# Kernel optimization log

Hardware: AMD Instinct MI355X
Metric: run time of the kernel (lower is better)

## Reference

```python
import jax, jax.numpy as jnp
import numpy as np
from jax import lax

N, M, B = 512, 1024, 1024  # signal dim, atoms, batch (batch==m required by X = W @ Gamma)
POWER_ITER = 100
IHT_ITER = 50


def setup_inputs() -> dict:
    key = jax.random.key(0)
    k1, k2 = jax.random.split(key)
    Y = jax.random.normal(k1, (B, N), dtype=jnp.float32)
    W = jax.random.normal(k2, (N, M), dtype=jnp.float32)
    return {"Y": Y, "W": W, "K": 64}


def power_method(W):
    # 100 iterations of X <- X W^T W / ||.||; returns last pre-normalization norm
    # (approx largest eigenvalue of W^T W), matching PowerMethod in the source.
    X0 = jax.random.normal(jax.random.key(42), (1, W.shape[1]), dtype=W.dtype)

    def body(i, carry):
        X, _ = carry
        X2 = (X @ W.T) @ W          # [1, m]
        nm = jnp.linalg.norm(X2)
        return (X2 / nm, nm)

    _, nm = lax.fori_loop(0, POWER_ITER, body, (X0, jnp.asarray(1.0, W.dtype)))
    return nm


def hard_threshold_k(G, K):
    # keep entries strictly larger (in abs) than the (K+1)-th largest per row
    a = jnp.sort(jnp.abs(G), axis=1)[:, ::-1]   # descending per row
    T = a[:, K][:, None]                          # [B, 1]
    return G * (jnp.abs(G) > T).astype(G.dtype)


def reference(Y, W, K):
    # NormDict: column-normalize the dictionary
    W = W / jnp.linalg.norm(W, axis=0)
    c = power_method(W)
    eta = 1.0 / c
    Yn = jnp.linalg.norm(Y)

    # IHT sparse coding
    Gamma = hard_threshold_k(Y @ (eta * W), K)     # [B, m]
    residual = Gamma @ W.T - Y                      # [B, n]

    def step(carry, _):
        Gamma, residual = carry
        Gamma = hard_threshold_k(Gamma - eta * (residual @ W), K)
        residual = Gamma @ W.T - Y
        return (Gamma, residual), jnp.linalg.norm(residual) / Yn

    (Gamma, residual), norms = lax.scan(step, (Gamma, residual), None, length=IHT_ITER)

    X = W @ Gamma  # [n, m] @ [B, m] -> requires B == m, as in the torch source
    return X, Gamma, norms
```

## Files before the change

### kernel.cpp

```cpp
#include <hip/hip_runtime.h>


#define DEV __device__ __forceinline__

constexpr int Nd = 512;
constexpr int Md = 1024;
constexpr int Bd = 1024;
constexpr int Ksp = 64;
constexpr int IHT = 50;

DEV float wave_reduce_f(float v) {
#pragma unroll
  for (int off = 32; off > 0; off >>= 1) v += __shfl_down(v, off);
  return v;
}
DEV double wave_reduce_d(double v) {
#pragma unroll
  for (int off = 32; off > 0; off >>= 1) v += __shfl_down(v, off);
  return v;
}
DEV float rfl_f(float v) {
  return __uint_as_float(__builtin_amdgcn_readfirstlane(__float_as_uint(v)));
}

__global__ void k_zero(double* dacc, int* pcnt) {
  int t = threadIdx.x;
  if (t < 51) dacc[t] = 0.0;
  if (t < 52) pcnt[t] = 0;
}

__global__ __launch_bounds__(256) void k_colnorm(const float* __restrict__ W,
                                                 float* __restrict__ cnorm) {
  int col = blockIdx.x * 256 + threadIdx.x;
  double ss = 0.0;
  for (int i = 0; i < Nd; ++i) {
    float w = W[(size_t)i * Md + col];
    ss = fma((double)w, (double)w, ss);
  }
  cnorm[col] = (float)sqrt(ss);
}

__global__ __launch_bounds__(256) void k_normalize(const float* __restrict__ W,
                                                   const float* __restrict__ cnorm,
                                                   float* __restrict__ Wn) {
  int idx = blockIdx.x * 256 + threadIdx.x;
  Wn[idx] = W[idx] / cnorm[idx & (Md - 1)];
}

__global__ __launch_bounds__(256) void k_yn2(const float* __restrict__ Y,
                                             double* __restrict__ dacc) {
  double s = 0.0;
  for (int i = blockIdx.x * 256 + threadIdx.x; i < Bd * Nd; i += gridDim.x * 256) {
    float y = Y[i];
    s = fma((double)y, (double)y, s);
  }
  s = wave_reduce_d(s);
  __shared__ double red[4];
  int lane = threadIdx.x & 63, wid = threadIdx.x >> 6;
  if (lane == 0) red[wid] = s;
  __syncthreads();
  if (threadIdx.x == 0) atomicAdd(&dacc[0], red[0] + red[1] + red[2] + red[3]);
}

template <int BM, int BN, int TN>
__global__ __launch_bounds__(256) void k_gemm_t(const float* __restrict__ A, int lda, int ta,
                                                const float* __restrict__ B, int ldb, int tb,
                                                float* __restrict__ C, int ldc, int Kd,
                                                float scale) {
  constexpr int AE = 32 * BM / 256;
  constexpr int BE = 32 * BN / 256;
  __shared__ __align__(16) float As[32][BM + 4];
  __shared__ __align__(16) float Bs[32][BN + 4];
  const int tid = threadIdx.x;
  const int tx = tid % (BN / TN), ty = tid / (BN / TN);
  const int m0 = blockIdx.y * BM, n0 = blockIdx.x * BN;
  float ra[AE], rb[BE];
  float acc[4][TN];
#pragma unroll
  for (int i = 0; i < 4; ++i)
#pragma unroll
    for (int j = 0; j < TN; ++j) acc[i][j] = 0.f;

  auto loadA = [&](int k0) {
    if (!ta) {
      const int c = tid & 31, r0 = tid >> 5;
#pragma unroll
      for (int i = 0; i < AE; ++i)
        ra[i] = A[(size_t)(m0 + r0 + i * 8) * lda + (k0 + c)];
    } else {
      const int r = tid % BM, c0 = tid / BM;
#pragma unroll
      for (int i = 0; i < AE; ++i)
        ra[i] = A[(size_t)(k0 + c0 + i * (256 / BM)) * lda + (m0 + r)];
    }
  };
  auto storeA = [&]() {
    if (!ta) {
      const int c = tid & 31, r0 = tid >> 5;
#pragma unroll
      for (int i = 0; i < AE; ++i) As[c][r0 + i * 8] = ra[i];
    } else {
      const int r = tid % BM, c0 = tid / BM;
#pragma unroll
      for (int i = 0; i < AE; ++i) As[c0 + i * (256 / BM)][r] = ra[i];
    }
  };
  auto loadB = [&](int k0) {
    if (!tb) {
      const int c = tid % BN, r0 = tid / BN;
#pragma unroll
      for (int i = 0; i < BE; ++i)
        rb[i] = B[(size_t)(k0 + r0 + i * (256 / BN)) * ldb + (n0 + c)];
    } else {
      const int r = tid & 31, c0 = tid >> 5;
#pragma unroll
      for (int i = 0; i < BE; ++i)
        rb[i] = B[(size_t)(n0 + c0 + i * 8) * ldb + (k0 + r)];
    }
  };
  auto storeB = [&]() {
    if (!tb) {
      const int c = tid % BN, r0 = tid / BN;
#pragma unroll
      for (int i = 0; i < BE; ++i) Bs[r0 + i * (256 / BN)][c] = rb[i];
    } else {
      const int r = tid & 31, c0 = tid >> 5;
#pragma unroll
      for (int i = 0; i < BE; ++i) Bs[r][c0 + i * 8] = rb[i];
    }
  };

  loadA(0);
  loadB(0);
  storeA();
  storeB();
  __syncthreads();
  for (int k0 = 0; k0 < Kd; k0 += 32) {
    const bool more = (k0 + 32) < Kd;
    if (more) { loadA(k0 + 32); loadB(k0 + 32); }
#pragma unroll
    for (int kk = 0; kk < 32; ++kk) {
      const float4 a4 = *(const float4*)&As[kk][ty * 4];
      const float aa[4] = {a4.x, a4.y, a4.z, a4.w};
      float bb[TN];
      if constexpr (TN == 4) {
        const float4 b4 = *(const float4*)&Bs[kk][tx * 4];
        bb[0] = b4.x; bb[1] = b4.y; bb[2] = b4.z; bb[3] = b4.w;
      } else {
        const float2 b2 = *(const float2*)&Bs[kk][tx * 2];
        bb[0] = b2.x; bb[1] = b2.y;
      }
#pragma unroll
      for (int i = 0; i < 4; ++i)
#pragma unroll
        for (int j = 0; j < TN; ++j) acc[i][j] = fmaf(aa[i], bb[j], acc[i][j]);
    }
    if (more) {
      __syncthreads();
      storeA();
      storeB();
      __syncthreads();
    }
  }
#pragma unroll
  for (int i = 0; i < 4; ++i) {
    if constexpr (TN == 4) {
      float4 o;
      o.x = acc[i][0] * scale; o.y = acc[i][1] * scale;
      o.z = acc[i][2] * scale; o.w = acc[i][3] * scale;
      *(float4*)&C[(size_t)(m0 + ty * 4 + i) * ldc + n0 + tx * 4] = o;
    } else {
      float2 o;
      o.x = acc[i][0] * scale; o.y = acc[i][1] * scale;
      *(float2*)&C[(size_t)(m0 + ty * 4 + i) * ldc + n0 + tx * 2] = o;
    }
  }
}

DEV float erfinv_xla(float x) {
  float w = -log1pf(-x * x);
  float p;
  if (w < 5.0f) {
    w = w - 2.5f;
    p = 2.81022636e-08f;
    p = fmaf(p, w, 3.43273939e-07f);
    p = fmaf(p, w, -3.5233877e-06f);
    p = fmaf(p, w, -4.39150654e-06f);
    p = fmaf(p, w, 0.00021858087f);
    p = fmaf(p, w, -0.00125372503f);
    p = fmaf(p, w, -0.00417768164f);
    p = fmaf(p, w, 0.246640727f);
    p = fmaf(p, w, 1.50140941f);
  } else {
    w = sqrtf(w) - 3.0f;
    p = -0.000200214257f;
    p = fmaf(p, w, 0.000100950558f);
    p = fmaf(p, w, 0.00134934322f);
    p = fmaf(p, w, -0.00367342844f);
    p = fmaf(p, w, 0.00573950773f);
    p = fmaf(p, w, -0.0076224613f);
    p = fmaf(p, w, 0.00943887047f);
    p = fmaf(p, w, 1.00167406f);
    p = fmaf(p, w, 2.83297682f);
  }
  return p * x;
}

#define TF_ROUND(r)                                  \
  {                                                  \
    x0 += x1;                                        \
    x1 = (x1 << (r)) | (x1 >> (32 - (r)));           \
    x1 ^= x0;                                        \
  }

__global__ __launch_bounds__(512) void k_power(const float* __restrict__ Wn,
                                               const float* __restrict__ S2,
                                               const float* __restrict__ Smat,
                                               float* __restrict__ V,
                                               float* __restrict__ cbuf,
                                               int* __restrict__ pcnt) {
  __shared__ float xbuf[Md];
  __shared__ double r99[8], r100[8];
  const int t = threadIdx.x, lane = t & 63, wv = t >> 6;
  const int bk = blockIdx.x;
  const int nblk = (int)gridDim.x;

  {
    unsigned i = (unsigned)t;
    unsigned x0 = i, x1 = i + 512u;
    const unsigned ks0 = 0u, ks1 = 42u, ks2 = 0x1BD11BDAu ^ 42u;
    x0 += ks0; x1 += ks1;
    TF_ROUND(13) TF_ROUND(15) TF_ROUND(26) TF_ROUND(6)  x0 += ks1; x1 += ks2 + 1u;
    TF_ROUND(17) TF_ROUND(29) TF_ROUND(16) TF_ROUND(24) x0 += ks2; x1 += ks0 + 2u;
    TF_ROUND(13) TF_ROUND(15) TF_ROUND(26) TF_ROUND(6)  x0 += ks0; x1 += ks1 + 3u;
    TF_ROUND(17) TF_ROUND(29) TF_ROUND(16) TF_ROUND(24) x0 += ks1; x1 += ks2 + 4u;
    TF_ROUND(13) TF_ROUND(15) TF_ROUND(26) TF_ROUND(6)  x0 += ks2; x1 += ks0 + 5u;
    const float lo = -0.99999994f;
    const float sqrt2 = 1.41421356237f;
    {
      float f = __uint_as_float((x0 >> 9) | 0x3f800000u) - 1.0f;
      float u = fmaxf(lo, f * 2.0f + lo);
      xbuf[i] = sqrt2 * erfinv_xla(u);
    }
    {
      float f = __uint_as_float((x1 >> 9) | 0x3f800000u) - 1.0f;
      float u = fmaxf(lo, f * 2.0f + lo);
      xbuf[i + 512] = sqrt2 * erfinv_xla(u);
    }
  }
  __syncthreads();

  float* s0 = V;
  float* s1 = V + 512;
  float* v99 = V + 1024;
  float* v100 = V + 1536;
  const int w = bk * 8 + wv;

  for (int i = 0; i < 8; ++i) {
    const int row = w + 64 * i;
    const float4* wr = (const float4*)(Wn + (size_t)row * Md);
    const float4* x4 = (const float4*)xbuf;
    float s = 0.f;
#pragma unroll
    for (int e = 0; e < 4; ++e) {
      const float4 w4 = wr[lane + e * 64];
      const float4 xx = x4[lane + e * 64];
      s = fmaf(w4.x, xx.x, s); s = fmaf(w4.y, xx.y, s);
      s = fmaf(w4.z, xx.z, s); s = fmaf(w4.w, xx.w, s);
    }
    s = wave_reduce_f(s);
    if (lane == 0) s0[row] = s;
  }
  __syncthreads();
  if (t == 0) {
    __hip_atomic_fetch_add(&pcnt[0], 1, __ATOMIC_RELEASE, __HIP_MEMORY_SCOPE_AGENT);
    while (__hip_atomic_load(&pcnt[0], __ATOMIC_ACQUIRE, __HIP_MEMORY_SCOPE_AGENT) < nblk) {}
  }
  __syncthreads();

  const float* pin = s0;
  for (int step = 0; step < 51; ++step) {
    const float* M;
    float scale;
    float* dst;
    if (step < 49)      { M = S2;   scale = 1.0f;   dst = (step & 1) ? s0 : s1; }
    else if (step == 49){ M = Smat; scale = 0.125f; dst = v99; }
    else                { M = Smat; scale = 0.125f; dst = v100; }
    for (int i = 0; i < 8; ++i) {
      const int row = w + 64 * i;
      const float4* mr = (const float4*)(M + (size_t)row * Nd);
      const float4* v4 = (const float4*)pin;
      float s = 0.f;
#pragma unroll
      for (int e = 0; e < 2; ++e) {
        const float4 m4 = mr[lane + e * 64];
        const float4 xx = v4[lane + e * 64];
        s = fmaf(m4.x, xx.x, s); s = fmaf(m4.y, xx.y, s);
        s = fmaf(m4.z, xx.z, s); s = fmaf(m4.w, xx.w, s);
      }
      s = wave_reduce_f(s);
      if (lane == 0) dst[row] = s * scale;
    }
    __syncthreads();
    if (t == 0) {
      __hip_atomic_fetch_add(&pcnt[1 + step], 1, __ATOMIC_RELEASE, __HIP_MEMORY_SCOPE_AGENT);
      while (__hip_atomic_load(&pcnt[1 + step], __ATOMIC_ACQUIRE, __HIP_MEMORY_SCOPE_AGENT) < nblk) {}
    }
    __syncthreads();
    pin = dst;
  }

  if (bk == 0) {
    double a = (double)v99[t]; a *= a;
    double b2 = (double)v100[t]; b2 *= b2;
    a = wave_reduce_d(a);
    b2 = wave_reduce_d(b2);
    if (lane == 0) { r99[wv] = a; r100[wv] = b2; }
    __syncthreads();
    if (t == 0) {
      double n99 = 0.0, n100 = 0.0;
      for (int i = 0; i < 8; ++i) { n99 += r99[i]; n100 += r100[i]; }
      float c = (float)(8.0 * sqrt(n100 / n99));
      cbuf[0] = c;
      cbuf[1] = 1.0f / c;
    }
  }
}

__global__ __launch_bounds__(256, 4) void k_iht_all(
    const float* __restrict__ Q, const float* __restrict__ YW,
    const float* __restrict__ cbuf, float* __restrict__ gdense,
    double* __restrict__ normacc) {
  __shared__ float u[Md];
  __shared__ float yws[Md];
  __shared__ float sval[Ksp];
  __shared__ int sidx[Ksp];
  __shared__ unsigned histbuf[2][4][256];
  __shared__ unsigned wred[4];
  __shared__ unsigned sel_need, sel_prefix;
  __shared__ double dred[4];
  __shared__ int scnt;

  const int t = threadIdx.x;
  const int b = blockIdx.x;
  const int lane = t & 63, wv = t >> 6;
  const float eta = cbuf[1];
  const float4 yw = ((const float4*)(YW + (size_t)b * Md))[t];
  ((float4*)yws)[t] = yw;
#pragma unroll
  for (int e = 0; e < 8; ++e) ((unsigned*)histbuf)[t + e * 256] = 0u;
  const float* Qt = Q + t * 4;

  for (int it = -1; it < IHT; ++it) {
    if (it >= 0) {
      const int cnt = scnt;
      float4 p = make_float4(0.f, 0.f, 0.f, 0.f);
      int k = 0;
      for (; k + 16 <= cnt; k += 16) {
        int ids[16];
        float gs[16];
        float4 qq[16];
#pragma unroll
        for (int j = 0; j < 16; ++j) {
          ids[j] = __builtin_amdgcn_readfirstlane(sidx[k + j]);
          gs[j] = rfl_f(sval[k + j]);
        }
#pragma unroll
        for (int j = 0; j < 16; ++j) qq[j] = *(const float4*)(Qt + (size_t)ids[j] * Md);
#pragma unroll
        for (int j = 0; j < 16; ++j) p.x = fmaf(gs[j], qq[j].x, p.x);
#pragma unroll
        for (int j = 0; j < 16; ++j) p.y = fmaf(gs[j], qq[j].y, p.y);
#pragma unroll
        for (int j = 0; j < 16; ++j) p.z = fmaf(gs[j], qq[j].z, p.z);
#pragma unroll
        for (int j = 0; j < 16; ++j) p.w = fmaf(gs[j], qq[j].w, p.w);
      }
      for (; k < cnt; ++k) {
        const int id = __builtin_amdgcn_readfirstlane(sidx[k]);
        const float g = rfl_f(sval[k]);
        const float4 q = *(const float4*)(Qt + (size_t)id * Md);
        p.x = fmaf(g, q.x, p.x); p.y = fmaf(g, q.y, p.y);
        p.z = fmaf(g, q.z, p.z); p.w = fmaf(g, q.w, p.w);
      }
      ((float4*)u)[t] = p;
      __syncthreads();
      if (it >= 1) {
        double part = 0.0;
        if (t < cnt) {
          const int id = sidx[t];
          part = (double)sval[t] * ((double)u[id] - 2.0 * (double)yws[id]);
        }
        part = wave_reduce_d(part);
        if (lane == 0) dred[wv] = part;
      }
      __syncthreads();
      if (it >= 1 && t == 0)
        atomicAdd(&normacc[it - 1], dred[0] + dred[1] + dred[2] + dred[3]);
      float4 uu;
      uu.x = -(eta * (p.x - yw.x)); uu.y = -(eta * (p.y - yw.y));
      uu.z = -(eta * (p.z - yw.z)); uu.w = -(eta * (p.w - yw.w));
      ((float4*)u)[t] = uu;
      __syncthreads();
      if (t < cnt) u[sidx[t]] += sval[t];
      __syncthreads();
    } else {
      float4 uu;
      uu.x = eta * yw.x; uu.y = eta * yw.y; uu.z = eta * yw.z; uu.w = eta * yw.w;
      ((float4*)u)[t] = uu;
      __syncthreads();
    }

    float vals[4];
    unsigned key[4];
    {
      const float4 mv = ((const float4*)u)[t];
      vals[0] = mv.x; vals[1] = mv.y; vals[2] = mv.z; vals[3] = mv.w;
#pragma unroll
      for (int e = 0; e < 4; ++e) key[e] = __float_as_uint(vals[e]) & 0x7fffffffu;
    }

    unsigned need = Ksp + 1, prefix = 0u, pmask = 0u;
#pragma unroll
    for (int pass = 3; pass >= 0; --pass) {
      const int sh = 8 * pass;
      const int pb = pass & 1;
      unsigned(*hist)[256] = histbuf[pb];
#pragma unroll
      for (int e = 0; e < 4; ++e)
        if ((key[e] & pmask) == prefix) atomicAdd(&hist[wv][(key[e] >> sh) & 255u], 1u);
      __syncthreads();
      unsigned* hz = histbuf[pb ^ 1][wv];
      hz[lane] = 0u; hz[lane + 64] = 0u; hz[lane + 128] = 0u; hz[lane + 192] = 0u;
      if (wv == 0) {
        const unsigned c0 = hist[0][lane] + hist[1][lane] + hist[2][lane] + hist[3][lane];
        const unsigned c1 = hist[0][lane + 64] + hist[1][lane + 64] + hist[2][lane + 64] + hist[3][lane + 64];
        const unsigned c2 = hist[0][lane + 128] + hist[1][lane + 128] + hist[2][lane + 128] + hist[3][lane + 128];
        const unsigned c3 = hist[0][lane + 192] + hist[1][lane + 192] + hist[2][lane + 192] + hist[3][lane + 192];
        unsigned s0 = c0, s1 = c1, s2 = c2, s3 = c3;
#pragma unroll
        for (int off = 1; off < 64; off <<= 1) {
          const unsigned y0 = __shfl_down(s0, off), y1 = __shfl_down(s1, off);
          const unsigned y2 = __shfl_down(s2, off), y3 = __shfl_down(s3, off);
          if (lane + off < 64) { s0 += y0; s1 += y1; s2 += y2; s3 += y3; }
        }
        const unsigned T1 = __builtin_amdgcn_readfirstlane(s1);
        const unsigned T2 = __builtin_amdgcn_readfirstlane(s2);
        const unsigned T3 = __builtin_amdgcn_readfirstlane(s3);
        const unsigned i0 = s0 + T1 + T2 + T3;
        const unsigned i1 = s1 + T2 + T3;
        const unsigned i2 = s2 + T3;
        const unsigned i3 = s3;
        if (i0 >= need && i0 - c0 < need) { sel_prefix = prefix | ((unsigned)lane << sh); sel_need = need - (i0 - c0); }
        if (i1 >= need && i1 - c1 < need) { sel_prefix = prefix | ((unsigned)(lane + 64) << sh); sel_need = need - (i1 - c1); }
        if (i2 >= need && i2 - c2 < need) { sel_prefix = prefix | ((unsigned)(lane + 128) << sh); sel_need = need - (i2 - c2); }
        if (i3 >= need && i3 - c3 < need) { sel_prefix = prefix | ((unsigned)(lane + 192) << sh); sel_need = need - (i3 - c3); }
      }
      __syncthreads();
      prefix = sel_prefix;
      need = sel_need;
      pmask |= (255u << sh);
    }
    const unsigned Tbits = prefix;

    unsigned keep = 0u;
    unsigned myc = 0u;
#pragma unroll
    for (int e = 0; e < 4; ++e)
      if (key[e] > Tbits) { keep |= (1u << e); ++myc; }
    unsigned x = myc;
#pragma unroll
    for (int off = 1; off < 64; off <<= 1) {
      const unsigned y = __shfl_up(x, off);
      if (lane >= off) x += y;
    }
    if (lane == 63) wred[wv] = x;
    __syncthreads();
    unsigned addlo = 0u;
    for (int w2 = 0; w2 < wv; ++w2) addlo += wred[w2];
    int base = (int)(x + addlo) - (int)myc;
#pragma unroll
    for (int e = 0; e < 4; ++e) {
      if (keep & (1u << e)) {
        sidx[base] = t * 4 + e;
        sval[base] = vals[e];
        ++base;
      }
    }
    if (t == 0) scnt = (int)(wred[0] + wred[1] + wred[2] + wred[3]);
    if (it == IHT - 1) {
      float4 g;
      g.x = (keep & 1u) ? vals[0] : 0.f;
      g.y = (keep & 2u) ? vals[1] : 0.f;
      g.z = (keep & 4u) ? vals[2] : 0.f;
      g.w = (keep & 8u) ? vals[3] : 0.f;
      ((float4*)(gdense + (size_t)b * Md))[t] = g;
    }
    __syncthreads();
  }

  const int cnt = scnt;
  if (wv == 0) {
    double part = 0.0;
    if (lane < cnt) {
      const int id = sidx[lane];
      float acc2 = 0.f;
      for (int k = 0; k < cnt; ++k)
        acc2 = fmaf(sval[k], Q[(size_t)sidx[k] * Md + id], acc2);
      part = (double)sval[lane] * ((double)acc2 - 2.0 * (double)yws[id]);
    }
    part = wave_reduce_d(part);
    if (lane == 0) atomicAdd(&normacc[IHT - 1], part);
  }
}

__global__ void k_wnorms(const double* __restrict__ dacc, float* __restrict__ onorms) {
  const int t = threadIdx.x;
  if (t < IHT) {
    const double yn2 = dacc[0];
    double r2 = yn2 + dacc[1 + t];
    if (r2 < 0.0) r2 = 0.0;
    onorms[t] = (float)(sqrt(r2) / sqrt(yn2));
  }
}

extern "C" void kernel_launch(void* const* d_in, const int* in_sizes, int n_in,
                              void* d_out, int out_size, void* d_ws, size_t ws_size,
                              hipStream_t stream) {
  (void)in_sizes; (void)n_in; (void)out_size; (void)ws_size;
  const float* Y = (const float*)d_in[0];
  const float* W = (const float*)d_in[1];
  float* out = (float*)d_out;
  float* outX = out;
  float* outG = out + Nd * Md;
  float* outN = outG + Bd * Md;

  char* wsb = (char*)d_ws;
  double* dacc = (double*)wsb;
  float* cbuf = (float*)(wsb + 512);
  float* Wn = (float*)(wsb + 1024);
  float* Q = Wn + Nd * Md;
  float* YW = Q + Md * Md;
  float* Smat = YW + Bd * Md;
  float* S2 = Smat + Nd * Nd;
  float* cnorm = S2 + Nd * Nd;
  float* V = cnorm + Md;
  int* pcnt = (int*)(V + 2048);

  k_zero<<<1, 64, 0, stream>>>(dacc, pcnt);
  k_colnorm<<<4, 256, 0, stream>>>(W, cnorm);
  k_normalize<<<2048, 256, 0, stream>>>(W, cnorm, Wn);

  k_gemm_t<64, 32, 2><<<dim3(16, 8), 256, 0, stream>>>(Wn, Md, 0, Wn, Md, 1, Smat, Nd, Md, 1.0f);
  k_gemm_t<64, 32, 2><<<dim3(16, 8), 256, 0, stream>>>(Smat, Nd, 0, Smat, Nd, 0, S2, Nd, Nd, 0.015625f);
  k_gemm_t<64, 64, 4><<<dim3(16, 16), 256, 0, stream>>>(Wn, Md, 1, Wn, Md, 0, Q, Md, Nd, 1.0f);
  k_gemm_t<64, 64, 4><<<dim3(16, 16), 256, 0, stream>>>(Y, Nd, 0, Wn, Md, 0, YW, Md, Nd, 1.0f);
  k_yn2<<<128, 256, 0, stream>>>(Y, dacc);

  k_power<<<8, 512, 0, stream>>>(Wn, S2, Smat, V, cbuf, pcnt);

  k_iht_all<<<1024, 256, 0, stream>>>(Q, YW, cbuf, outG, dacc + 1);
  k_wnorms<<<1, 64, 0, stream>>>(dacc, outN);

  k_gemm_t<64, 32, 2><<<dim3(32, 8), 256, 0, stream>>>(Wn, Md, 0, outG, Md, 0, outX, Md, Md, 1.0f);
}
```

Measured before the change: 1.066 ms.

## Replace atomic-counter grid barrier with per-block flags and double power blocks

The persistent power-iteration kernel now uses a flag-based grid barrier. Each block publishes a monotonically increasing step value in its own padded slot, and one wavefront polls all slots with a wave-wide vote. This replaces a shared atomic counter per step. The block count goes from 8 to 16, so each wave handles 4 rows instead of 8, aiming to shorten each of the 51 serialized steps. The trade-off is more blocks taking part in every barrier, and the zeroing kernel is widened to clear the padded flag array.

```diff
diff --git a/kernel.cpp b/kernel.cpp
--- a/kernel.cpp
+++ b/kernel.cpp
@@ -8,6 +8,7 @@
 constexpr int Bd = 1024;
 constexpr int Ksp = 64;
 constexpr int IHT = 50;
+constexpr int NBLK = 16;
 
 DEV float wave_reduce_f(float v) {
 #pragma unroll
@@ -23,10 +24,10 @@
   return __uint_as_float(__builtin_amdgcn_readfirstlane(__float_as_uint(v)));
 }
 
-__global__ void k_zero(double* dacc, int* pcnt) {
+__global__ __launch_bounds__(512) void k_zero(double* dacc, int* pcnt) {
   int t = threadIdx.x;
   if (t < 51) dacc[t] = 0.0;
-  if (t < 52) pcnt[t] = 0;
+  pcnt[t] = 0;
 }
 
 __global__ __launch_bounds__(256) void k_colnorm(const float* __restrict__ W,
@@ -223,7 +224,24 @@
   __shared__ double r99[8], r100[8];
   const int t = threadIdx.x, lane = t & 63, wv = t >> 6;
   const int bk = blockIdx.x;
-  const int nblk = (int)gridDim.x;
+
+  auto flag_barrier = [&](int val) {
+    __syncthreads();
+    if (t == 0)
+      __hip_atomic_store(&pcnt[bk * 32], val, __ATOMIC_RELEASE,
+                         __HIP_MEMORY_SCOPE_AGENT);
+    if (wv == 0) {
+      while (true) {
+        int f = (lane < NBLK)
+                    ? __hip_atomic_load(&pcnt[lane * 32], __ATOMIC_ACQUIRE,
+                                        __HIP_MEMORY_SCOPE_AGENT)
+                    : val;
+        if (__all(f >= val)) break;
+        __builtin_amdgcn_s_sleep(1);
+      }
+    }
+    __syncthreads();
+  };
 
   {
     unsigned i = (unsigned)t;
@@ -255,9 +273,11 @@
   float* v99 = V + 1024;
   float* v100 = V + 1536;
   const int w = bk * 8 + wv;
-
-  for (int i = 0; i < 8; ++i) {
-    const int row = w + 64 * i;
+  constexpr int NW = NBLK * 8;
+  constexpr int RPW = 512 / NW;
+
+  for (int i = 0; i < RPW; ++i) {
+    const int row = w + NW * i;
     const float4* wr = (const float4*)(Wn + (size_t)row * Md);
     const float4* x4 = (const float4*)xbuf;
     float s = 0.f;
@@ -271,12 +291,7 @@
     s = wave_reduce_f(s);
     if (lane == 0) s0[row] = s;
   }
-  __syncthreads();
-  if (t == 0) {
-    __hip_atomic_fetch_add(&pcnt[0], 1, __ATOMIC_RELEASE, __HIP_MEMORY_SCOPE_AGENT);
-    while (__hip_atomic_load(&pcnt[0], __ATOMIC_ACQUIRE, __HIP_MEMORY_SCOPE_AGENT) < nblk) {}
-  }
-  __syncthreads();
+  flag_barrier(1);
 
   const float* pin = s0;
   for (int step = 0; step < 51; ++step) {
@@ -286,8 +301,8 @@
     if (step < 49)      { M = S2;   scale = 1.0f;   dst = (step & 1) ? s0 : s1; }
     else if (step == 49){ M = Smat; scale = 0.125f; dst = v99; }
     else                { M = Smat; scale = 0.125f; dst = v100; }
-    for (int i = 0; i < 8; ++i) {
-      const int row = w + 64 * i;
+    for (int i = 0; i < RPW; ++i) {
+      const int row = w + NW * i;
       const float4* mr = (const float4*)(M + (size_t)row * Nd);
       const float4* v4 = (const float4*)pin;
       float s = 0.f;
@@ -301,12 +316,7 @@
       s = wave_reduce_f(s);
       if (lane == 0) dst[row] = s * scale;
     }
-    __syncthreads();
-    if (t == 0) {
-      __hip_atomic_fetch_add(&pcnt[1 + step], 1, __ATOMIC_RELEASE, __HIP_MEMORY_SCOPE_AGENT);
-      while (__hip_atomic_load(&pcnt[1 + step], __ATOMIC_ACQUIRE, __HIP_MEMORY_SCOPE_AGENT) < nblk) {}
-    }
-    __syncthreads();
+    flag_barrier(step + 2);
     pin = dst;
   }
 
@@ -547,7 +557,7 @@
   float* V = cnorm + Md;
   int* pcnt = (int*)(V + 2048);
 
-  k_zero<<<1, 64, 0, stream>>>(dacc, pcnt);
+  k_zero<<<1, 512, 0, stream>>>(dacc, pcnt);
   k_colnorm<<<4, 256, 0, stream>>>(W, cnorm);
   k_normalize<<<2048, 256, 0, stream>>>(W, cnorm, Wn);
 
@@ -557,7 +567,7 @@
   k_gemm_t<64, 64, 4><<<dim3(16, 16), 256, 0, stream>>>(Y, Nd, 0, Wn, Md, 0, YW, Md, Nd, 1.0f);
   k_yn2<<<128, 256, 0, stream>>>(Y, dacc);
 
-  k_power<<<8, 512, 0, stream>>>(Wn, S2, Smat, V, cbuf, pcnt);
+  k_power<<<NBLK, 512, 0, stream>>>(Wn, S2, Smat, V, cbuf, pcnt);
 
   k_iht_all<<<1024, 256, 0, stream>>>(Q, YW, cbuf, outG, dacc + 1);
   k_wnorms<<<1, 64, 0, stream>>>(dacc, outN);
```

Result: faster. 1.010 ms (-5.2%).
